# Kernel optimization log

Measured on AMD Instinct MI355X. Metric: run time of the kernel, lower is better.

Reference implementation:

```python
import jax, jax.numpy as jnp
from jax import lax
import numpy as np

B = 512

def setup_inputs() -> dict:
    key = jax.random.key(0)
    ks = jax.random.split(key, 6)
    x = jax.random.normal(ks[0], (B, 1, 28, 28), jnp.float32)
    conv1_w = jax.random.normal(ks[1], (256, 1, 9, 9), jnp.float32) * 0.05
    conv1_b = jnp.zeros((256,), jnp.float32)
    prim_w = jax.random.normal(ks[2], (32, 32, 1, 9, 9), jnp.float32) * 0.02
    prim_b = jnp.zeros((32,), jnp.float32)
    dig_W = jax.random.normal(ks[3], (1152, 8, 16), jnp.float32) * 0.1
    dig_Wb = jnp.zeros((1152, 16), jnp.float32)
    out_w = jax.random.normal(ks[4], (10, 10, 16, 1), jnp.float32) * 0.1
    out_b = jnp.zeros((10,), jnp.float32)
    return dict(x=x, conv1_w=conv1_w, conv1_b=conv1_b, prim_w=prim_w, prim_b=prim_b,
                dig_W=dig_W, dig_Wb=dig_Wb, out_w=out_w, out_b=out_b)


def _squash(s):
    # s: [B, 16, 10]; matches torch: v = ||s||_2/(1+||s||_2) * (s^T / ||s||_1)
    l2 = jnp.sqrt(jnp.sum(s * s, axis=1))[:, :, None]      # [B, 10, 1]
    l1 = jnp.sum(jnp.abs(s), axis=1)[:, :, None]            # [B, 10, 1]
    return l2 / (1.0 + l2) * (jnp.swapaxes(s, 1, 2) / l1)   # [B, 10, 16]


def reference(x, conv1_w, conv1_b, prim_w, prim_b, dig_W, dig_Wb, out_w, out_b):
    # conv1: [B,1,28,28] -> [B,256,20,20]
    out = lax.conv_general_dilated(x, conv1_w, (1, 1), 'VALID',
                                   dimension_numbers=('NCHW', 'OIHW', 'NCHW'))
    out = jax.nn.relu(out + conv1_b[None, :, None, None])
    # primary capsules: [B,32,8,20,20] -> [B,32,8,6,6]
    out1 = out.reshape(-1, 32, 8, 20, 20)
    out1 = lax.conv_general_dilated(out1, prim_w, (1, 2, 2), 'VALID',
                                    dimension_numbers=('NCDHW', 'OIDHW', 'NCDHW'))
    out1 = jax.nn.relu(out1 + prim_b[None, :, None, None, None])
    # transpose(2,-1) then reshape -> [B, 1152, 8]
    u = jnp.swapaxes(out1, 2, 4).reshape(-1, 1152, 8)
    # per-capsule affine: [B,1152,16]
    dig = jnp.einsum('bnd,nde->bne', u, dig_W) + dig_Wb
    bsz = dig.shape[0]
    # dynamic routing: b logits are never updated in the source, so
    # c = softmax(zeros, dim=1) = 1/1152 uniform, and all 3 iterations produce
    # the identical v. Computed once (same math as the original loop).
    c = jnp.full((bsz, 1152, 10), 1.0 / 1152, dtype=dig.dtype)
    s = jnp.einsum('bni,bnd->bdi', c, dig)   # [B, 16, 10]
    v = _squash(s)                            # [B, 10, 16]
    # output Conv2d(10,10,[16,1]) on v[...,None] reduces fully -> [B,10]
    logits = jnp.einsum('bik,oik->bo', v, out_w[..., 0]) + out_b
    return jax.nn.softmax(logits, axis=1)
```

## Files before the change

### kernel.cpp

```cpp
#include <hip/hip_runtime.h>
#include <math.h>


typedef __attribute__((ext_vector_type(8))) short bf16x8;
typedef __attribute__((ext_vector_type(4))) float f32x4;

__device__ inline unsigned short f2bf(float f) {
    union { float f; unsigned u; } v; v.f = f;
    unsigned r = v.u + 0x7fff + ((v.u >> 16) & 1);
    return (unsigned short)(r >> 16);
}

#define C1TN 16008

__global__ void caps_pre(const float* __restrict__ conv1_w,
                         const float* __restrict__ prim_w,
                         const float* __restrict__ dig_Wb,
                         const float* __restrict__ out_w,
                         float* __restrict__ S,
                         float* __restrict__ colsum,
                         float* __restrict__ OW,
                         unsigned short* __restrict__ c1wp2,
                         unsigned short* __restrict__ pw2,
                         int B)
{
    const int t = threadIdx.x;
    if (blockIdx.x == 468) {
        __shared__ float cs[16];
        if (t < 16) cs[t] = 0.f;
        __syncthreads();
        {
            const int k = t & 15, g = t >> 4;
            float s = 0.f;
            for (int j = 0; j < 72; ++j) s += dig_Wb[(g * 72 + j) * 16 + k];
            atomicAdd(&cs[k], s);
        }
        __syncthreads();
        if (t < 16) colsum[t] = cs[t];
        if (t >= 64 && t < 224) {
            const int idx = t - 64, o = idx >> 4, k = idx & 15;
            float s = 0.f;
            for (int i = 0; i < 10; ++i) s += out_w[(o * 10 + i) * 16 + k];
            OW[idx] = s;
        }
        return;
    }
    const int tid = blockIdx.x * 256 + t;
    if (tid < 24576) {
        const int c = tid / 96, kn = tid % 96;
        unsigned short v = 0;
        if (kn < 72) {
            const int p = kn >> 1, lo = kn & 1, ky = p >> 2, kx = 2 * (p & 3) + lo;
            v = f2bf(conv1_w[c * 81 + 9 * ky + kx]);
        } else if (kn < 81) {
            v = f2bf(conv1_w[c * 81 + 9 * (kn - 72) + 8]);
        }
        c1wp2[tid] = v;
    } else if (tid < 24576 + 87040) {
        const int j = tid - 24576;
        const int t81 = j >> 10, rem = j & 1023, o = rem >> 5, i = rem & 31;
        pw2[j] = (t81 < 81) ? f2bf(prim_w[(o * 32 + i) * 81 + t81]) : (unsigned short)0;
    } else {
        const int k = tid - 111616;
        if (k < B * 16) S[k] = 0.f;
    }
}

__global__ __launch_bounds__(256, 2) void caps_main(
    const float* __restrict__ x,
    const float* __restrict__ conv1_b,
    const float* __restrict__ prim_b,
    const float* __restrict__ dig_W,
    const unsigned short* __restrict__ c1wp2,
    const unsigned short* __restrict__ pw2,
    float* __restrict__ S)
{
    __shared__ __align__(16) unsigned short c1t[2 * C1TN];
    __shared__ __align__(16) unsigned imgp[1344];
    __shared__ unsigned short offT[64];
    __shared__ float pbs[32];

    const int b = blockIdx.x >> 2, dp = blockIdx.x & 3;
    const int d0 = dp * 2;
    const int t = threadIdx.x;
    const int wave = t >> 6, lane = t & 63, quad = lane >> 4, l16 = lane & 15;

    const float* xb = x + b * 784;
    for (int j = t; j < 1344; j += 256) {
        unsigned v = 0;
        if (j < 784) {
            const float a = xb[j];
            const int xc = j - 28 * (int)(((unsigned)j * 37450u) >> 20);
            const float c = (xc < 27) ? xb[j + 1] : 0.f;
            v = (unsigned)f2bf(a) | ((unsigned)f2bf(c) << 16);
        }
        imgp[j] = v;
    }
    if (t < 64) {
        int v;
        if (t < 32) {
            const int ky = t >> 2, kx = 2 * (t & 3);
            v = ky * 28 + kx;
        } else {
            const int k = t + 32;
            if (k < 72) {
                const int p = k >> 1, lo = k & 1, ky = p >> 2, kx = 2 * (p & 3) + lo;
                v = ky * 28 + kx;
            } else if (k < 81) {
                v = (k - 72) * 28 + 8;
            } else v = 784;
        }
        offT[t] = (unsigned short)(4 * v);
    }
    if (t < 32) pbs[t] = prim_b[t];
    __syncthreads();

    unsigned tp0[4], tp1[4], t2a[4], t2b[4];
#pragma unroll
    for (int r = 0; r < 4; ++r) {
        tp0[r] = offT[quad * 4 + r];
        tp1[r] = offT[16 + quad * 4 + r];
        t2a[r] = offT[32 + quad * 8 + 2 * r];
        t2b[r] = offT[32 + quad * 8 + 2 * r + 1];
    }

    {
        const int e = wave >> 1;
        const int d = d0 + e;
        unsigned short* dst = c1t + e * C1TN;
        const float cb0 = conv1_b[l16 * 8 + d];
        const float cb1 = conv1_b[(16 + l16) * 8 + d];
        bf16x8 Bw0[3], Bw1[3];
#pragma unroll
        for (int ks = 0; ks < 3; ++ks) {
            Bw0[ks] = *(const bf16x8*)&c1wp2[(l16 * 8 + d) * 96 + ks * 32 + quad * 8];
            Bw1[ks] = *(const bf16x8*)&c1wp2[((16 + l16) * 8 + d) * 96 + ks * 32 + quad * 8];
        }
        for (int mt = (wave & 1); mt < 25; mt += 2) {
            const int pos = mt * 16 + l16;
            const int y = (int)(((unsigned)pos * 52429u) >> 20);
            const unsigned pb4 = (unsigned)(pos + 8 * y) * 4u;
            f32x4 a0 = {0.f, 0.f, 0.f, 0.f}, a1 = {0.f, 0.f, 0.f, 0.f};
            union { unsigned u[4]; bf16x8 v; } A;
#pragma unroll
            for (int r = 0; r < 4; ++r)
                A.u[r] = *(const unsigned*)((const char*)imgp + (pb4 + tp0[r]));
            a0 = __builtin_amdgcn_mfma_f32_16x16x32_bf16(A.v, Bw0[0], a0, 0, 0, 0);
            a1 = __builtin_amdgcn_mfma_f32_16x16x32_bf16(A.v, Bw1[0], a1, 0, 0, 0);
#pragma unroll
            for (int r = 0; r < 4; ++r)
                A.u[r] = *(const unsigned*)((const char*)imgp + (pb4 + tp1[r]));
            a0 = __builtin_amdgcn_mfma_f32_16x16x32_bf16(A.v, Bw0[1], a0, 0, 0, 0);
            a1 = __builtin_amdgcn_mfma_f32_16x16x32_bf16(A.v, Bw1[1], a1, 0, 0, 0);
#pragma unroll
            for (int r = 0; r < 4; ++r) {
                const unsigned lo = *(const unsigned*)((const char*)imgp + (pb4 + t2a[r]));
                const unsigned hi = *(const unsigned*)((const char*)imgp + (pb4 + t2b[r]));
                A.u[r] = (lo & 0xFFFFu) | (hi << 16);
            }
            a0 = __builtin_amdgcn_mfma_f32_16x16x32_bf16(A.v, Bw0[2], a0, 0, 0, 0);
            a1 = __builtin_amdgcn_mfma_f32_16x16x32_bf16(A.v, Bw1[2], a1, 0, 0, 0);
#pragma unroll
            for (int r = 0; r < 4; ++r) {
                const int pr = mt * 16 + quad * 4 + r;
                const int spar = (int)((((unsigned)pr * 52429u) >> 21) & 1u);
                const int base = pr * 40 + 8 * spar;
                dst[base + l16]      = f2bf(fmaxf(a0[r] + cb0, 0.f));
                dst[base + 16 + l16] = f2bf(fmaxf(a1[r] + cb1, 0.f));
            }
        }
    }
    __syncthreads();

    const int hp = l16 >> 3, wp = l16 & 7;
    const unsigned Lbase = 80u * (unsigned)(40 * hp + 2 * wp) + 16u * quad;
    const unsigned Lh0 = Lbase + 16u * hp;
    const unsigned Lh1 = Lbase + 16u * (1 - hp);

    f32x4 pa[12];
#pragma unroll
    for (int q = 0; q < 12; ++q) pa[q] = (f32x4){0.f, 0.f, 0.f, 0.f};

    {
        const unsigned short* apbase = pw2 + l16 * 32 + quad * 8;
        int off = wave;
        bf16x8 A0 = *(const bf16x8*)(apbase + off * 1024);
        bf16x8 A1 = *(const bf16x8*)(apbase + off * 1024 + 512);
        for (; off < 81; off += 4) {
            const int noff = off + 4;
            const bf16x8 nA0 = *(const bf16x8*)(apbase + noff * 1024);
            const bf16x8 nA1 = *(const bf16x8*)(apbase + noff * 1024 + 512);
            const int ky = (off * 57) >> 9;
            const int kx = off - 9 * ky;
            const int kk = (ky >> 1) & 1;
            const unsigned soff = 80u * (unsigned)(20 * ky + kx);
            const unsigned ad = (kk ? Lh1 : Lh0) + soff;
            const char* b0 = (const char*)c1t + ad;
#pragma unroll
            for (int nt = 0; nt < 3; ++nt) {
                const bf16x8 Bf0 = *(const bf16x8*)(b0 + nt * 6400);
                const bf16x8 Bf1 = *(const bf16x8*)(b0 + nt * 6400 + 2 * C1TN);
                pa[nt]     = __builtin_amdgcn_mfma_f32_16x16x32_bf16(A0, Bf0, pa[nt],     0, 0, 0);
                pa[3 + nt] = __builtin_amdgcn_mfma_f32_16x16x32_bf16(A1, Bf0, pa[3 + nt], 0, 0, 0);
                pa[6 + nt] = __builtin_amdgcn_mfma_f32_16x16x32_bf16(A0, Bf1, pa[6 + nt], 0, 0, 0);
                pa[9 + nt] = __builtin_amdgcn_mfma_f32_16x16x32_bf16(A1, Bf1, pa[9 + nt], 0, 0, 0);
            }
            A0 = nA0; A1 = nA1;
        }
    }
    __syncthreads();

    f32x4* redbuf = (f32x4*)c1t;
    if (wave >= 2) {
#pragma unroll
        for (int q = 0; q < 12; ++q) redbuf[((wave - 2) * 12 + q) * 64 + lane] = pa[q];
    }
    __syncthreads();
    if (wave < 2) {
#pragma unroll
        for (int q = 0; q < 12; ++q) pa[q] += redbuf[(wave * 12 + q) * 64 + lane];
        if (wave == 0) {
#pragma unroll
            for (int q = 0; q < 6; ++q) redbuf[(24 + q) * 64 + lane] = pa[6 + q];
        } else {
#pragma unroll
            for (int q = 0; q < 6; ++q) redbuf[(30 + q) * 64 + lane] = pa[q];
        }
    }
    __syncthreads();

    if (wave < 2) {
        const int d = d0 + wave;
        f32x4 full[6];
#pragma unroll
        for (int q = 0; q < 6; ++q)
            full[q] = (wave == 0) ? (pa[q] + redbuf[(30 + q) * 64 + lane])
                                  : (pa[6 + q] + redbuf[(24 + q) * 64 + lane]);

        float part[16];
#pragma unroll
        for (int k = 0; k < 16; ++k) part[k] = 0.f;

        if (wp < 6) {
#pragma unroll
            for (int mt = 0; mt < 2; ++mt)
#pragma unroll
                for (int nt = 0; nt < 3; ++nt) {
                    const f32x4 u4 = full[mt * 3 + nt];
                    const int h = 2 * nt + hp;
#pragma unroll
                    for (int r = 0; r < 4; ++r) {
                        const int o = mt * 16 + quad * 4 + r;
                        const float val = fmaxf(u4[r] + pbs[o], 0.f);
                        const int nc = o * 36 + wp * 6 + h;
                        const f32x4* wd = (const f32x4*)&dig_W[(nc * 8 + d) * 16];
#pragma unroll
                        for (int m = 0; m < 4; ++m) {
                            const f32x4 wv = wd[m];
                            part[m * 4 + 0] = fmaf(val, wv[0], part[m * 4 + 0]);
                            part[m * 4 + 1] = fmaf(val, wv[1], part[m * 4 + 1]);
                            part[m * 4 + 2] = fmaf(val, wv[2], part[m * 4 + 2]);
                            part[m * 4 + 3] = fmaf(val, wv[3], part[m * 4 + 3]);
                        }
                    }
                }
        }

#pragma unroll
        for (int k = 0; k < 16; ++k) {
            float v = part[k];
            v += __shfl_xor(v, 32, 64);
            v += __shfl_xor(v, 16, 64);
            v += __shfl_xor(v, 8, 64);
            v += __shfl_xor(v, 4, 64);
            v += __shfl_xor(v, 2, 64);
            v += __shfl_xor(v, 1, 64);
            part[k] = v;
        }
        if (lane == 0) {
#pragma unroll
            for (int k = 0; k < 16; ++k) atomicAdd(&S[b * 16 + k], part[k]);
        }
    }
}

__global__ void caps_epi(const float* __restrict__ S, const float* __restrict__ colsum,
                         const float* __restrict__ OW, const float* __restrict__ out_b,
                         float* __restrict__ out, int B)
{
    const int b = blockIdx.x * 256 + threadIdx.x;
    if (b >= B) return;
    float Sv[16]; float l2 = 0.f, l1 = 0.f;
#pragma unroll
    for (int k = 0; k < 16; ++k) {
        const float s = (S[b * 16 + k] + colsum[k]) * (1.f / 1152.f);
        Sv[k] = s; l2 += s * s; l1 += fabsf(s);
    }
    l2 = sqrtf(l2);
    const float sc = l2 / (1.f + l2) / l1;
    float lg[10]; float mx = -1e30f;
#pragma unroll
    for (int o = 0; o < 10; ++o) {
        float a = out_b[o];
#pragma unroll
        for (int k = 0; k < 16; ++k) a = fmaf(Sv[k] * sc, OW[o * 16 + k], a);
        lg[o] = a; mx = fmaxf(mx, a);
    }
    float sum = 0.f;
#pragma unroll
    for (int o = 0; o < 10; ++o) { lg[o] = expf(lg[o] - mx); sum += lg[o]; }
    const float inv = 1.f / sum;
#pragma unroll
    for (int o = 0; o < 10; ++o) out[b * 10 + o] = lg[o] * inv;
}

extern "C" void kernel_launch(void* const* d_in, const int* in_sizes, int n_in,
                              void* d_out, int out_size, void* d_ws, size_t ws_size,
                              hipStream_t stream) {
    const float* x       = (const float*)d_in[0];
    const float* conv1_w = (const float*)d_in[1];
    const float* conv1_b = (const float*)d_in[2];
    const float* prim_w  = (const float*)d_in[3];
    const float* prim_b  = (const float*)d_in[4];
    const float* dig_W   = (const float*)d_in[5];
    const float* dig_Wb  = (const float*)d_in[6];
    const float* out_w   = (const float*)d_in[7];
    const float* out_b   = (const float*)d_in[8];
    float* out = (float*)d_out;

    const int B = in_sizes[0] / 784;

    char* w = (char*)d_ws;
    float* S              = (float*)(w);
    float* colsum         = (float*)(w + 32768);
    float* OW             = (float*)(w + 32832);
    unsigned short* c1wp2 = (unsigned short*)(w + 33472);
    unsigned short* pw2   = (unsigned short*)(w + 33472 + 49152);

    caps_pre<<<469, 256, 0, stream>>>(conv1_w, prim_w, dig_Wb, out_w,
                                      S, colsum, OW, c1wp2, pw2, B);
    caps_main<<<B * 4, 256, 0, stream>>>(x, conv1_b, prim_b, dig_W, c1wp2, pw2, S);
    caps_epi<<<(B + 255) / 256, 256, 0, stream>>>(S, colsum, OW, out_b, out, B);
}
```

Measured before the change: 182.1 us.

## Fuse epilogue into main kernel via last-block counter; transpose image for tap loads

Result: slower. 199.5 us (+9.5%).

```diff
diff --git a/kernel.cpp b/kernel.cpp
--- a/kernel.cpp
+++ b/kernel.cpp
@@ -20,6 +20,7 @@
                          float* __restrict__ S,
                          float* __restrict__ colsum,
                          float* __restrict__ OW,
+                         unsigned* __restrict__ done,
                          unsigned short* __restrict__ c1wp2,
                          unsigned short* __restrict__ pw2,
                          int B)
@@ -28,6 +29,7 @@
     if (blockIdx.x == 468) {
         __shared__ float cs[16];
         if (t < 16) cs[t] = 0.f;
+        if (t == 255) *done = 0u;
         __syncthreads();
         {
             const int k = t & 15, g = t >> 4;
@@ -56,13 +58,13 @@
             v = f2bf(conv1_w[c * 81 + 9 * (kn - 72) + 8]);
         }
         c1wp2[tid] = v;
-    } else if (tid < 24576 + 87040) {
+    } else if (tid < 111616) {
         const int j = tid - 24576;
-        const int t81 = j >> 10, rem = j & 1023, o = rem >> 5, i = rem & 31;
-        pw2[j] = (t81 < 81) ? f2bf(prim_w[(o * 32 + i) * 81 + t81]) : (unsigned short)0;
+        const int tap = j >> 10, rem = j & 1023, o = rem >> 5, ipos = rem & 31;
+        const int ch = (ipos >> 1) | ((ipos & 1) << 4);
+        pw2[j] = (tap < 81) ? f2bf(prim_w[(o * 32 + ch) * 81 + tap]) : (unsigned short)0;
     } else {
-        const int k = tid - 111616;
-        if (k < B * 16) S[k] = 0.f;
+        S[tid - 111616] = 0.f;
     }
 }
 
@@ -73,12 +75,19 @@
     const float* __restrict__ dig_W,
     const unsigned short* __restrict__ c1wp2,
     const unsigned short* __restrict__ pw2,
-    float* __restrict__ S)
+    float* __restrict__ S,
+    const float* __restrict__ colsum,
+    const float* __restrict__ OW,
+    const float* __restrict__ out_b,
+    unsigned* __restrict__ done,
+    float* __restrict__ out,
+    int nblocks)
 {
     __shared__ __align__(16) unsigned short c1t[2 * C1TN];
-    __shared__ __align__(16) unsigned imgp[1344];
-    __shared__ unsigned short offT[64];
+    __shared__ __align__(16) unsigned imgp[2148];
+    __shared__ unsigned short offT[32];
     __shared__ float pbs[32];
+    __shared__ int lastflag;
 
     const int b = blockIdx.x >> 2, dp = blockIdx.x & 3;
     const int d0 = dp * 2;
@@ -86,43 +95,42 @@
     const int wave = t >> 6, lane = t & 63, quad = lane >> 4, l16 = lane & 15;
 
     const float* xb = x + b * 784;
-    for (int j = t; j < 1344; j += 256) {
+    for (int j = t; j < 2148; j += 256) {
         unsigned v = 0;
         if (j < 784) {
             const float a = xb[j];
             const int xc = j - 28 * (int)(((unsigned)j * 37450u) >> 20);
             const float c = (xc < 27) ? xb[j + 1] : 0.f;
             v = (unsigned)f2bf(a) | ((unsigned)f2bf(c) << 16);
+        } else if (j < 1568) {
+            const int m = j - 784;
+            const int xx = (int)(((unsigned)m * 37450u) >> 20);
+            const int yy = m - 28 * xx;
+            const float a = xb[yy * 28 + xx];
+            const float c = (yy < 27) ? xb[(yy + 1) * 28 + xx] : 0.f;
+            v = (unsigned)f2bf(a) | ((unsigned)f2bf(c) << 16);
         }
         imgp[j] = v;
     }
-    if (t < 64) {
-        int v;
-        if (t < 32) {
-            const int ky = t >> 2, kx = 2 * (t & 3);
-            v = ky * 28 + kx;
-        } else {
-            const int k = t + 32;
-            if (k < 72) {
-                const int p = k >> 1, lo = k & 1, ky = p >> 2, kx = 2 * (p & 3) + lo;
-                v = ky * 28 + kx;
-            } else if (k < 81) {
-                v = (k - 72) * 28 + 8;
-            } else v = 784;
-        }
-        offT[t] = (unsigned short)(4 * v);
-    }
-    if (t < 32) pbs[t] = prim_b[t];
-    __syncthreads();
-
-    unsigned tp0[4], tp1[4], t2a[4], t2b[4];
+    if (t < 32) {
+        const int ky = t >> 2, kx = 2 * (t & 3);
+        offT[t] = (unsigned short)(4 * (ky * 28 + kx));
+        pbs[t] = prim_b[t];
+    }
+    if (t == 0) lastflag = 0;
+    __syncthreads();
+
+    unsigned tp0[4], tp1[4], s2off[4];
 #pragma unroll
     for (int r = 0; r < 4; ++r) {
         tp0[r] = offT[quad * 4 + r];
         tp1[r] = offT[16 + quad * 4 + r];
-        t2a[r] = offT[32 + quad * 8 + 2 * r];
-        t2b[r] = offT[32 + quad * 8 + 2 * r + 1];
-    }
+        s2off[r] = (quad == 0) ? 4u * (224 + 2 * r)
+                 : (quad == 1) ? 4u * (1008 + 2 * r)
+                 : (quad == 2 && r == 0) ? 4u * 1016
+                 : 4u * 1596;
+    }
+    const unsigned mkA = (quad == 2) ? 0x0000FFFFu : 0xFFFFFFFFu;
 
     {
         const int e = wave >> 1;
@@ -139,7 +147,10 @@
         for (int mt = (wave & 1); mt < 25; mt += 2) {
             const int pos = mt * 16 + l16;
             const int y = (int)(((unsigned)pos * 52429u) >> 20);
-            const unsigned pb4 = (unsigned)(pos + 8 * y) * 4u;
+            const int x2 = pos - 20 * y;
+            const unsigned pb4 = (unsigned)(y * 28 + x2) * 4u;
+            const unsigned qb4 = (unsigned)(x2 * 28 + y) * 4u;
+            const unsigned bks2 = (quad == 0) ? pb4 : qb4;
             f32x4 a0 = {0.f, 0.f, 0.f, 0.f}, a1 = {0.f, 0.f, 0.f, 0.f};
             union { unsigned u[4]; bf16x8 v; } A;
 #pragma unroll
@@ -153,11 +164,9 @@
             a0 = __builtin_amdgcn_mfma_f32_16x16x32_bf16(A.v, Bw0[1], a0, 0, 0, 0);
             a1 = __builtin_amdgcn_mfma_f32_16x16x32_bf16(A.v, Bw1[1], a1, 0, 0, 0);
 #pragma unroll
-            for (int r = 0; r < 4; ++r) {
-                const unsigned lo = *(const unsigned*)((const char*)imgp + (pb4 + t2a[r]));
-                const unsigned hi = *(const unsigned*)((const char*)imgp + (pb4 + t2b[r]));
-                A.u[r] = (lo & 0xFFFFu) | (hi << 16);
-            }
+            for (int r = 0; r < 4; ++r)
+                A.u[r] = *(const unsigned*)((const char*)imgp + (bks2 + s2off[r]));
+            A.u[0] &= mkA;
             a0 = __builtin_amdgcn_mfma_f32_16x16x32_bf16(A.v, Bw0[2], a0, 0, 0, 0);
             a1 = __builtin_amdgcn_mfma_f32_16x16x32_bf16(A.v, Bw1[2], a1, 0, 0, 0);
 #pragma unroll
@@ -165,8 +174,9 @@
                 const int pr = mt * 16 + quad * 4 + r;
                 const int spar = (int)((((unsigned)pr * 52429u) >> 21) & 1u);
                 const int base = pr * 40 + 8 * spar;
-                dst[base + l16]      = f2bf(fmaxf(a0[r] + cb0, 0.f));
-                dst[base + 16 + l16] = f2bf(fmaxf(a1[r] + cb1, 0.f));
+                const unsigned pk = (unsigned)f2bf(fmaxf(a0[r] + cb0, 0.f))
+                                  | ((unsigned)f2bf(fmaxf(a1[r] + cb1, 0.f)) << 16);
+                *(unsigned*)&dst[base + 2 * l16] = pk;
             }
         }
     }
@@ -282,36 +292,43 @@
             for (int k = 0; k < 16; ++k) atomicAdd(&S[b * 16 + k], part[k]);
         }
     }
-}
-
-__global__ void caps_epi(const float* __restrict__ S, const float* __restrict__ colsum,
-                         const float* __restrict__ OW, const float* __restrict__ out_b,
-                         float* __restrict__ out, int B)
-{
-    const int b = blockIdx.x * 256 + threadIdx.x;
-    if (b >= B) return;
-    float Sv[16]; float l2 = 0.f, l1 = 0.f;
-#pragma unroll
-    for (int k = 0; k < 16; ++k) {
-        const float s = (S[b * 16 + k] + colsum[k]) * (1.f / 1152.f);
-        Sv[k] = s; l2 += s * s; l1 += fabsf(s);
-    }
-    l2 = sqrtf(l2);
-    const float sc = l2 / (1.f + l2) / l1;
-    float lg[10]; float mx = -1e30f;
-#pragma unroll
-    for (int o = 0; o < 10; ++o) {
-        float a = out_b[o];
-#pragma unroll
-        for (int k = 0; k < 16; ++k) a = fmaf(Sv[k] * sc, OW[o * 16 + k], a);
-        lg[o] = a; mx = fmaxf(mx, a);
-    }
-    float sum = 0.f;
-#pragma unroll
-    for (int o = 0; o < 10; ++o) { lg[o] = expf(lg[o] - mx); sum += lg[o]; }
-    const float inv = 1.f / sum;
-#pragma unroll
-    for (int o = 0; o < 10; ++o) out[b * 10 + o] = lg[o] * inv;
+
+    __asm__ volatile("s_waitcnt vmcnt(0)" ::: "memory");
+    __syncthreads();
+
+    if (t == 0) {
+        const unsigned old = atomicAdd(done, 1u);
+        lastflag = (old == (unsigned)(nblocks - 1)) ? 1 : 0;
+    }
+    __syncthreads();
+    if (lastflag) {
+        const int nimg = nblocks >> 2;
+        for (int bb = t; bb < nimg; bb += 256) {
+            float Sv[16]; float l2 = 0.f, l1 = 0.f;
+#pragma unroll
+            for (int k = 0; k < 16; ++k) {
+                const float sv = atomicAdd(&S[bb * 16 + k], 0.0f);
+                const float s = (sv + colsum[k]) * (1.f / 1152.f);
+                Sv[k] = s; l2 += s * s; l1 += fabsf(s);
+            }
+            l2 = sqrtf(l2);
+            const float sc = l2 / (1.f + l2) / l1;
+            float lg[10]; float mx = -1e30f;
+#pragma unroll
+            for (int o = 0; o < 10; ++o) {
+                float a = out_b[o];
+#pragma unroll
+                for (int k = 0; k < 16; ++k) a = fmaf(Sv[k] * sc, OW[o * 16 + k], a);
+                lg[o] = a; mx = fmaxf(mx, a);
+            }
+            float sum = 0.f;
+#pragma unroll
+            for (int o = 0; o < 10; ++o) { lg[o] = expf(lg[o] - mx); sum += lg[o]; }
+            const float inv = 1.f / sum;
+#pragma unroll
+            for (int o = 0; o < 10; ++o) out[bb * 10 + o] = lg[o] * inv;
+        }
+    }
 }
 
 extern "C" void kernel_launch(void* const* d_in, const int* in_sizes, int n_in,
@@ -334,11 +351,13 @@
     float* S              = (float*)(w);
     float* colsum         = (float*)(w + 32768);
     float* OW             = (float*)(w + 32832);
-    unsigned short* c1wp2 = (unsigned short*)(w + 33472);
-    unsigned short* pw2   = (unsigned short*)(w + 33472 + 49152);
-
+    unsigned* done        = (unsigned*)(w + 33472);
+    unsigned short* c1wp2 = (unsigned short*)(w + 33536);
+    unsigned short* pw2   = (unsigned short*)(w + 33536 + 49152);
+
+    const int nblocks = B * 4;
     caps_pre<<<469, 256, 0, stream>>>(conv1_w, prim_w, dig_Wb, out_w,
-                                      S, colsum, OW, c1wp2, pw2, B);
-    caps_main<<<B * 4, 256, 0, stream>>>(x, conv1_b, prim_b, dig_W, c1wp2, pw2, S);
-    caps_epi<<<(B + 255) / 256, 256, 0, stream>>>(S, colsum, OW, out_b, out, B);
+                                      S, colsum, OW, done, c1wp2, pw2, B);
+    caps_main<<<nblocks, 256, 0, stream>>>(x, conv1_b, prim_b, dig_W, c1wp2, pw2,
+                                           S, colsum, OW, out_b, done, out, nblocks);
 }
```
